# Kernel tuning notes

Measured on AMD Instinct MI355X. Metric: run time of the kernel, lower is better.

Reference implementation:

```python
import jax, jax.numpy as jnp
import numpy as np

N_NODES = 50000
N_EDGES = 800000
VOCAB = 4096          # node_emb_size
EMB_DIM = 128         # node_emb_dim
HIDDEN = 128          # hidden_dim -> layer1 out = 2*HIDDEN
N_POS = 1024


def gcn_conv(h, edge_index, W, b, n):
    """PyG GCNConv: lin -> add self loops -> sym-normalized scatter-add -> +bias."""
    h = h @ W                                   # [N, out]
    row, col = edge_index[0], edge_index[1]     # source, target
    loop = jnp.arange(n)
    row = jnp.concatenate([row, loop])
    col = jnp.concatenate([col, loop])
    deg = jax.ops.segment_sum(jnp.ones(row.shape[0], dtype=h.dtype), col, num_segments=n)
    dinv = jnp.where(deg > 0, jax.lax.rsqrt(deg), 0.0)
    norm = dinv[row] * dinv[col]                # [E+N]
    msg = h[row] * norm[:, None]                # gather + scale
    return jax.ops.segment_sum(msg, col, num_segments=n) + b


def setup_inputs() -> dict:
    key = jax.random.key(0)
    ks = jax.random.split(key, 10)
    x = jax.random.randint(ks[0], (N_NODES, 1), 0, VOCAB)
    edge_index = jax.random.randint(ks[1], (2, N_EDGES), 0, N_NODES)
    x_position = jax.random.randint(ks[2], (N_POS,), 0, N_NODES)
    # Embedding init: normal(0, emb_dim^-0.5) per initialize_parameters
    emb = jax.random.normal(ks[3], (VOCAB, EMB_DIM), jnp.float32) * EMB_DIM ** -0.5
    # GCN / linear weights (glorot-ish)
    W1 = jax.random.normal(ks[4], (EMB_DIM, 2 * HIDDEN), jnp.float32) * (EMB_DIM ** -0.5)
    b1 = jnp.zeros((2 * HIDDEN,), jnp.float32)
    W2 = jax.random.normal(ks[5], (2 * HIDDEN, HIDDEN), jnp.float32) * ((2 * HIDDEN) ** -0.5)
    b2 = jnp.zeros((HIDDEN,), jnp.float32)
    Wc = jax.random.normal(ks[6], (HIDDEN, VOCAB), jnp.float32) * (HIDDEN ** -0.5)
    bc = jnp.zeros((VOCAB,), jnp.float32)
    return {"x": x, "edge_index": edge_index, "x_position": x_position,
            "emb": emb, "W1": W1, "b1": b1, "W2": W2, "b2": b2, "Wc": Wc, "bc": bc}


def reference(x, edge_index, x_position, emb, W1, b1, W2, b2, Wc, bc):
    n = x.shape[0]
    h = emb[x[:, 0]]                                   # Embedding + squeeze(1)
    h = jax.nn.relu(gcn_conv(h, edge_index, W1, b1, n))
    z = gcn_conv(h, edge_index, W2, b2, n)             # [N, HIDDEN]
    logits = z @ Wc + bc                               # classifier over all nodes
    # embedding stage: mean of classified rows at x_position, keep dim 0
    return jnp.mean(logits[x_position], axis=0, keepdims=True)  # [1, VOCAB]
```

## Files before the change

kernel.cpp:

```cpp
#include <hip/hip_runtime.h>

constexpr int EMB  = 128;
constexpr int H1D  = 256;
constexpr int H2D  = 128;
constexpr int VOC  = 4096;
constexpr int NSL  = 32;
constexpr int RPB  = 4;

constexpr int NRANGE = 8;
constexpr int TEAMS  = 128;
constexpr int RCAP   = 6400;
constexpr int HIST_B = NRANGE * TEAMS;
constexpr int GEMM_B = VOC / RPB;
constexpr int KB_GRID = HIST_B + GEMM_B;

__global__ void kA_init(int* count, unsigned int* flagbits, unsigned int* needw,
                        float* wagg, float* wsum, int* nflag, int* total,
                        const int* __restrict__ xpos,
                        int n, int nwords, int np) {
    int t = threadIdx.x;
    if (blockIdx.x == 0) {
        for (int i = t; i < nwords; i += 256) flagbits[i] = 0u;
        for (int i = t; i < n; i += 256) count[i] = 0;
        __syncthreads();
        for (int i = t; i < np; i += 256) {
            int v = xpos[i];
            atomicAdd(&count[v], 1);
            atomicOr(&flagbits[v >> 5], 1u << (v & 31));
        }
        if (t == 0) { *nflag = 0; *total = 0; }
    } else {
        const int stride = (gridDim.x - 1) * 256;
        const int i0 = (blockIdx.x - 1) * 256 + t;
        for (int i = i0; i < n; i += stride) wagg[i] = 0.0f;
        for (int i = i0; i < nwords; i += stride) needw[i] = 0u;
        for (int i = i0; i < NSL * H1D; i += stride) wsum[i] = 0.0f;
    }
}

__global__ __launch_bounds__(256) void kB_embW1_hist(
        const float* __restrict__ emb, const float* __restrict__ W1,
        float* __restrict__ embW1,
        const int* __restrict__ row, const int* __restrict__ col,
        const unsigned int* __restrict__ flagbits,
        unsigned short* __restrict__ cntp16, unsigned int* markw,
        int ne, int R, int sTeam) {
    __shared__ int sbuf[RCAP];
    int t = threadIdx.x;
    if (blockIdx.x < HIST_B) {
        int h     = blockIdx.x;
        int team  = h >> 3;
        int range = h & (NRANGE - 1);
        int base  = range * R;
        for (int i = t; i < R; i += 256) sbuf[i] = 0;
        __syncthreads();
        int q  = (((ne + TEAMS - 1) / TEAMS) + 255) & ~255;
        int e0 = team * q;
        int e1 = min(ne, e0 + q);
        for (int e = e0 + t; e < e1; e += 256) {
            int c = col[e];
            unsigned int d = (unsigned int)(c - base);
            if (d < (unsigned int)R) {
                atomicAdd(&sbuf[d], 1);
                if ((flagbits[c >> 5] >> (c & 31)) & 1u) {
                    int r = row[e];
                    atomicOr(&markw[r >> 5], 1u << (r & 31));
                }
            }
        }
        __syncthreads();
        unsigned short* outp = cntp16 + (size_t)team * sTeam + base;
        for (int i = t; i < R; i += 256) outp[i] = (unsigned short)sbuf[i];
    } else {
        float (*er)[EMB] = (float (*)[EMB])sbuf;
        int r0 = (blockIdx.x - HIST_B) * RPB;
        for (int i = t; i < RPB * EMB; i += 256)
            er[i / EMB][i % EMB] = emb[(size_t)r0 * EMB + i];
        __syncthreads();
        float acc[RPB];
#pragma unroll
        for (int rr = 0; rr < RPB; rr++) acc[rr] = 0.0f;
        for (int k = 0; k < EMB; k++) {
            float w = W1[k * H1D + t];
#pragma unroll
            for (int rr = 0; rr < RPB; rr++) acc[rr] += er[rr][k] * w;
        }
#pragma unroll
        for (int rr = 0; rr < RPB; rr++)
            embW1[(size_t)(r0 + rr) * H1D + t] = acc[rr];
    }
}

__global__ void k_alloc(unsigned int* needw,
                        const unsigned int* __restrict__ flagbits,
                        const unsigned short* __restrict__ cntp16,
                        const int* __restrict__ count,
                        const int* __restrict__ x,
                        float* wagg, int* needlist, int* nflag, int* total,
                        int* offs, int* cursor, int2* pk, int* cnt,
                        int n, int sTeam) {
    int v = blockIdx.x * blockDim.x + threadIdx.x;
    int lane = threadIdx.x & 63;
    int cv = 0;
    bool need = false;
    if (v < n) {
        const unsigned short* cp = cntp16 + v;
#pragma unroll 8
        for (int tt = 0; tt < TEAMS; tt++) cv += cp[(size_t)tt * sTeam];
        cnt[v] = cv;
        float dv = rsqrtf((float)cv + 1.0f);
        int2 p; p.x = x[v]; p.y = __float_as_int(dv);
        pk[v] = p;
        bool mark = (needw[v >> 5] >> (v & 31)) & 1u;
        bool flag = (flagbits[v >> 5] >> (v & 31)) & 1u;
        need = mark || flag;
        if (flag) wagg[v] = (float)count[v] / ((float)cv + 1.0f);
    }
    unsigned long long nm = __ballot(need);
    int wbase = (v & ~63) >> 5;
    if (lane == 0)  needw[wbase]     = (unsigned int)(nm & 0xffffffffu);
    if (lane == 32) needw[wbase + 1] = (unsigned int)(nm >> 32);
    int seg = need ? cv : 0;
    int incl = seg;
#pragma unroll
    for (int d = 1; d < 64; d <<= 1) {
        int t2 = __shfl_up(incl, d);
        if (lane >= d) incl += t2;
    }
    int excl = incl - seg;
    int wave_total = __shfl(incl, 63);
    int rank = __popcll(nm & ((1ull << lane) - 1));
    int wcnt = __popcll(nm);
    int base_id = 0, base_off = 0;
    if (lane == 0) {
        if (wcnt > 0)       base_id  = atomicAdd(nflag, wcnt);
        if (wave_total > 0) base_off = atomicAdd(total, wave_total);
    }
    base_id  = __shfl(base_id, 0);
    base_off = __shfl(base_off, 0);
    if (need) {
        needlist[base_id + rank] = v;
        int o = base_off + excl;
        offs[v] = o;
        cursor[v] = o;
    }
}

__global__ void k_scatter(const int* __restrict__ row, const int* __restrict__ col,
                          const unsigned int* __restrict__ needw,
                          const unsigned int* __restrict__ flagbits,
                          const int* __restrict__ count,
                          const int2* __restrict__ pk,
                          int* cursor, int2* srowp, float* wagg, int ne) {
    int e = blockIdx.x * blockDim.x + threadIdx.x;
    if (e < ne) {
        int c = col[e];
        if ((needw[c >> 5] >> (c & 31)) & 1u) {
            int r = row[e];
            int pos = atomicAdd(&cursor[c], 1);
            int2 pr = pk[r];
            srowp[pos] = pr;
            if ((flagbits[c >> 5] >> (c & 31)) & 1u) {
                float dc = __int_as_float(pk[c].y);
                float dr = __int_as_float(pr.y);
                atomicAdd(&wagg[r], (float)count[c] * dc * dr);
            }
        }
    }
}

__global__ void k_fconv(const int* __restrict__ needlist, const int* __restrict__ nneed_p,
                        const float* __restrict__ wagg, const int* __restrict__ x,
                        const int2* __restrict__ srowp,
                        const int* __restrict__ offs, const int* __restrict__ cnt,
                        const float* __restrict__ embW1, const float* __restrict__ b1,
                        float* __restrict__ wsum) {
    int lane = threadIdx.x & 63;
    int wib  = threadIdx.x >> 6;
    int wid  = blockIdx.x * (blockDim.x >> 6) + wib;
    int nw   = gridDim.x * (blockDim.x >> 6);
    int nn   = *nneed_p;
    const float4* __restrict__ ew = (const float4*)embW1;
    float4 bfrag = ((const float4*)b1)[lane];
    float4 acc2 = {0.0f, 0.0f, 0.0f, 0.0f};

    for (int i = wid; i < nn; i += nw) {
        int v = needlist[i];
        int cv = cnt[v];
        float dv = rsqrtf((float)cv + 1.0f);
        float wa = wagg[v];
        float4 s = ew[(size_t)x[v] * 64 + lane];
        float w0 = dv * dv;
        float4 acc;
        acc.x = bfrag.x + w0 * s.x;
        acc.y = bfrag.y + w0 * s.y;
        acc.z = bfrag.z + w0 * s.z;
        acc.w = bfrag.w + w0 * s.w;
        int start = offs[v], m = cv;
        for (int base = 0; base < m; base += 64) {
            int mm = min(64, m - base);
            int xr = 0; float wr = 0.0f;
            if (lane < mm) {
                int2 pk2 = srowp[start + base + lane];
                xr = pk2.x;
                wr = __int_as_float(pk2.y) * dv;
            }
            int e = 0;
            for (; e + 4 <= mm; e += 4) {
                int i0 = __shfl(xr, e),     i1 = __shfl(xr, e + 1);
                int i2 = __shfl(xr, e + 2), i3 = __shfl(xr, e + 3);
                float q0 = __shfl(wr, e),     q1 = __shfl(wr, e + 1);
                float q2 = __shfl(wr, e + 2), q3 = __shfl(wr, e + 3);
                float4 t0 = ew[(size_t)i0 * 64 + lane];
                float4 t1 = ew[(size_t)i1 * 64 + lane];
                float4 t2 = ew[(size_t)i2 * 64 + lane];
                float4 t3 = ew[(size_t)i3 * 64 + lane];
                acc.x += q0 * t0.x + q1 * t1.x + q2 * t2.x + q3 * t3.x;
                acc.y += q0 * t0.y + q1 * t1.y + q2 * t2.y + q3 * t3.y;
                acc.z += q0 * t0.z + q1 * t1.z + q2 * t2.z + q3 * t3.z;
                acc.w += q0 * t0.w + q1 * t1.w + q2 * t2.w + q3 * t3.w;
            }
            for (; e < mm; e++) {
                int i0 = __shfl(xr, e);
                float q0 = __shfl(wr, e);
                float4 t0 = ew[(size_t)i0 * 64 + lane];
                acc.x += q0 * t0.x;
                acc.y += q0 * t0.y;
                acc.z += q0 * t0.z;
                acc.w += q0 * t0.w;
            }
        }
        acc2.x += wa * fmaxf(acc.x, 0.0f);
        acc2.y += wa * fmaxf(acc.y, 0.0f);
        acc2.z += wa * fmaxf(acc.z, 0.0f);
        acc2.w += wa * fmaxf(acc.w, 0.0f);
    }

    __shared__ float red[4][H1D];
    red[wib][4 * lane + 0] = acc2.x;
    red[wib][4 * lane + 1] = acc2.y;
    red[wib][4 * lane + 2] = acc2.z;
    red[wib][4 * lane + 3] = acc2.w;
    __syncthreads();
    int t = threadIdx.x;
    float ssum = red[0][t] + red[1][t] + red[2][t] + red[3][t];
    atomicAdd(&wsum[(blockIdx.x & (NSL - 1)) * H1D + t], ssum);
}

__global__ void k_zout(const float* __restrict__ wsum, const float* __restrict__ W2,
                       const float* __restrict__ b2, const float* __restrict__ Wc,
                       const float* __restrict__ bc, float* __restrict__ out,
                       float inv_np) {
    __shared__ float ws[H1D];
    __shared__ float z[H2D];
    __shared__ float red[256];
    int t = threadIdx.x;
    float s = 0.0f;
#pragma unroll
    for (int c2 = 0; c2 < NSL; c2++) s += wsum[c2 * H1D + t];
    ws[t] = s;
    __syncthreads();
    if (t < H2D) {
        float acc = 0.0f;
#pragma unroll 8
        for (int k = 0; k < H1D; k++) acc += ws[k] * W2[k * H2D + t];
        z[t] = b2[t] + acc * inv_np;
    }
    __syncthreads();
    int c  = blockIdx.x * 64 + (t & 63);
    int ks = t >> 6;
    float acc = 0.0f;
#pragma unroll 8
    for (int j = ks * 32; j < ks * 32 + 32; j++) acc += z[j] * Wc[(size_t)j * VOC + c];
    red[t] = acc;
    __syncthreads();
    if (t < 64) {
        int cc = blockIdx.x * 64 + t;
        out[cc] = bc[cc] + red[t] + red[t + 64] + red[t + 128] + red[t + 192];
    }
}

extern "C" void kernel_launch(void* const* d_in, const int* in_sizes, int n_in,
                              void* d_out, int out_size, void* d_ws, size_t ws_size,
                              hipStream_t stream) {
    const int n  = in_sizes[0];
    const int ne = in_sizes[1] / 2;
    const int np = in_sizes[2];

    const int*   x    = (const int*)d_in[0];
    const int*   ei   = (const int*)d_in[1];
    const int*   xpos = (const int*)d_in[2];
    const float* emb  = (const float*)d_in[3];
    const float* W1   = (const float*)d_in[4];
    const float* b1   = (const float*)d_in[5];
    const float* W2   = (const float*)d_in[6];
    const float* b2   = (const float*)d_in[7];
    const float* Wc   = (const float*)d_in[8];
    const float* bc   = (const float*)d_in[9];
    float*       out  = (float*)d_out;

    const int* row = ei;
    const int* col = ei + ne;

    char* p = (char*)d_ws;
    auto alloc = [&](size_t bytes) {
        char* r = p;
        p += (bytes + 255) & ~(size_t)255;
        return r;
    };
    const int nb     = (n + 255) / 256;
    const int neb    = (ne + 255) / 256;
    const int nwords = nb * 8;
    const int R      = (n + NRANGE - 1) / NRANGE;
    const int sTeam  = NRANGE * R;

    int*            cnt      = (int*)alloc((size_t)n * 4);
    int*            offs     = (int*)alloc((size_t)n * 4);
    int*            cursor   = (int*)alloc((size_t)n * 4);
    int*            count    = (int*)alloc((size_t)n * 4);
    int*            needlist = (int*)alloc((size_t)n * 4);
    unsigned int*   needw    = (unsigned int*)alloc((size_t)nwords * 4);
    unsigned int*   flagbits = (unsigned int*)alloc((size_t)nwords * 4);
    int2*           srowp    = (int2*)alloc((size_t)ne * 8);
    int2*           pk       = (int2*)alloc((size_t)n * 8);
    unsigned short* cntp16   = (unsigned short*)alloc((size_t)TEAMS * sTeam * 2);
    int*            nflag    = (int*)alloc(256 * 4);
    int*            total    = (int*)alloc(256 * 4);
    float*          wagg     = (float*)alloc((size_t)n * 4);
    float*          embW1    = (float*)alloc((size_t)VOC * H1D * 4);
    float*          wsum     = (float*)alloc((size_t)NSL * H1D * 4);

    kA_init<<<nb, 256, 0, stream>>>(count, flagbits, needw, wagg, wsum,
                                    nflag, total, xpos, n, nwords, np);
    kB_embW1_hist<<<KB_GRID, 256, 0, stream>>>(emb, W1, embW1, row, col, flagbits,
                                               cntp16, needw, ne, R, sTeam);
    k_alloc<<<nb, 256, 0, stream>>>(needw, flagbits, cntp16, count, x, wagg,
                                    needlist, nflag, total, offs, cursor, pk, cnt,
                                    n, sTeam);
    k_scatter<<<neb, 256, 0, stream>>>(row, col, needw, flagbits, count, pk,
                                       cursor, srowp, wagg, ne);
    k_fconv<<<2048, 256, 0, stream>>>(needlist, nflag, wagg, x, srowp, offs, cnt,
                                      embW1, b1, wsum);
    k_zout<<<VOC / 64, 256, 0, stream>>>(wsum, W2, b2, Wc, bc, out, 1.0f / (float)np);
}
```

Measured before the change: 169.7 us.

## Pack histogram counters and edge payloads to 16-bit, halve teams, widen zout grid

The histogram now packs two 16-bit counters per shared-memory word with half as many teams, which halves the LDS footprint and the partial-count traffic. Per-node records shrink from int2 (vocab id plus dinv float) to one 32-bit word holding a 16-bit degree and a 16-bit vocab id, and dinv is recomputed with rsqrtf where needed. This halves gather and scatter bandwidth, but it assumes vocab ids and per-team counts fit in 16 bits. The classifier kernel is launched with 4x more blocks, each handling 16 columns, to raise parallelism over the Wc read.

New measurement: 179.2 us. 5.6% more time.

```diff
diff --git a/kernel.cpp b/kernel.cpp
--- a/kernel.cpp
+++ b/kernel.cpp
@@ -8,8 +8,8 @@
 constexpr int RPB  = 4;
 
 constexpr int NRANGE = 8;
-constexpr int TEAMS  = 128;
-constexpr int RCAP   = 6400;
+constexpr int TEAMS  = 64;
+constexpr int RCAPW  = 3200;
 constexpr int HIST_B = NRANGE * TEAMS;
 constexpr int GEMM_B = VOC / RPB;
 constexpr int KB_GRID = HIST_B + GEMM_B;
@@ -45,14 +45,15 @@
         const unsigned int* __restrict__ flagbits,
         unsigned short* __restrict__ cntp16, unsigned int* markw,
         int ne, int R, int sTeam) {
-    __shared__ int sbuf[RCAP];
+    __shared__ unsigned int sbuf[RCAPW];
     int t = threadIdx.x;
     if (blockIdx.x < HIST_B) {
         int h     = blockIdx.x;
         int team  = h >> 3;
         int range = h & (NRANGE - 1);
         int base  = range * R;
-        for (int i = t; i < R; i += 256) sbuf[i] = 0;
+        int RW    = R >> 1;
+        for (int i = t; i < RW; i += 256) sbuf[i] = 0u;
         __syncthreads();
         int q  = (((ne + TEAMS - 1) / TEAMS) + 255) & ~255;
         int e0 = team * q;
@@ -61,7 +62,7 @@
             int c = col[e];
             unsigned int d = (unsigned int)(c - base);
             if (d < (unsigned int)R) {
-                atomicAdd(&sbuf[d], 1);
+                atomicAdd(&sbuf[d >> 1], 1u << ((d & 1) << 4));
                 if ((flagbits[c >> 5] >> (c & 31)) & 1u) {
                     int r = row[e];
                     atomicOr(&markw[r >> 5], 1u << (r & 31));
@@ -69,8 +70,9 @@
             }
         }
         __syncthreads();
-        unsigned short* outp = cntp16 + (size_t)team * sTeam + base;
-        for (int i = t; i < R; i += 256) outp[i] = (unsigned short)sbuf[i];
+        unsigned int* outp32 =
+            (unsigned int*)(cntp16 + (size_t)team * sTeam + base);
+        for (int i = t; i < RW; i += 256) outp32[i] = sbuf[i];
     } else {
         float (*er)[EMB] = (float (*)[EMB])sbuf;
         int r0 = (blockIdx.x - HIST_B) * RPB;
@@ -97,7 +99,7 @@
                         const int* __restrict__ count,
                         const int* __restrict__ x,
                         float* wagg, int* needlist, int* nflag, int* total,
-                        int* offs, int* cursor, int2* pk, int* cnt,
+                        int* offs, int* cursor, unsigned int* pkc, int* cnt,
                         int n, int sTeam) {
     int v = blockIdx.x * blockDim.x + threadIdx.x;
     int lane = threadIdx.x & 63;
@@ -108,9 +110,7 @@
 #pragma unroll 8
         for (int tt = 0; tt < TEAMS; tt++) cv += cp[(size_t)tt * sTeam];
         cnt[v] = cv;
-        float dv = rsqrtf((float)cv + 1.0f);
-        int2 p; p.x = x[v]; p.y = __float_as_int(dv);
-        pk[v] = p;
+        pkc[v] = ((unsigned int)cv << 16) | (unsigned int)(x[v] & 0xFFFF);
         bool mark = (needw[v >> 5] >> (v & 31)) & 1u;
         bool flag = (flagbits[v >> 5] >> (v & 31)) & 1u;
         need = mark || flag;
@@ -150,19 +150,19 @@
                           const unsigned int* __restrict__ needw,
                           const unsigned int* __restrict__ flagbits,
                           const int* __restrict__ count,
-                          const int2* __restrict__ pk,
-                          int* cursor, int2* srowp, float* wagg, int ne) {
+                          const unsigned int* __restrict__ pkc,
+                          int* cursor, unsigned int* srow4, float* wagg, int ne) {
     int e = blockIdx.x * blockDim.x + threadIdx.x;
     if (e < ne) {
         int c = col[e];
         if ((needw[c >> 5] >> (c & 31)) & 1u) {
             int r = row[e];
             int pos = atomicAdd(&cursor[c], 1);
-            int2 pr = pk[r];
-            srowp[pos] = pr;
+            unsigned int pr = pkc[r];
+            srow4[pos] = pr;
             if ((flagbits[c >> 5] >> (c & 31)) & 1u) {
-                float dc = __int_as_float(pk[c].y);
-                float dr = __int_as_float(pr.y);
+                float dr = rsqrtf((float)(pr >> 16) + 1.0f);
+                float dc = rsqrtf((float)(pkc[c] >> 16) + 1.0f);
                 atomicAdd(&wagg[r], (float)count[c] * dc * dr);
             }
         }
@@ -171,7 +171,7 @@
 
 __global__ void k_fconv(const int* __restrict__ needlist, const int* __restrict__ nneed_p,
                         const float* __restrict__ wagg, const int* __restrict__ x,
-                        const int2* __restrict__ srowp,
+                        const unsigned int* __restrict__ srow4,
                         const int* __restrict__ offs, const int* __restrict__ cnt,
                         const float* __restrict__ embW1, const float* __restrict__ b1,
                         float* __restrict__ wsum) {
@@ -201,9 +201,9 @@
             int mm = min(64, m - base);
             int xr = 0; float wr = 0.0f;
             if (lane < mm) {
-                int2 pk2 = srowp[start + base + lane];
-                xr = pk2.x;
-                wr = __int_as_float(pk2.y) * dv;
+                unsigned int pk2 = srow4[start + base + lane];
+                xr = (int)(pk2 & 0xFFFFu);
+                wr = rsqrtf((float)(pk2 >> 16) + 1.0f) * dv;
             }
             int e = 0;
             for (; e + 4 <= mm; e += 4) {
@@ -267,16 +267,19 @@
         z[t] = b2[t] + acc * inv_np;
     }
     __syncthreads();
-    int c  = blockIdx.x * 64 + (t & 63);
-    int ks = t >> 6;
+    int c  = blockIdx.x * 16 + (t & 15);
+    int js = t >> 4;
     float acc = 0.0f;
-#pragma unroll 8
-    for (int j = ks * 32; j < ks * 32 + 32; j++) acc += z[j] * Wc[(size_t)j * VOC + c];
+#pragma unroll
+    for (int j = js * 8; j < js * 8 + 8; j++) acc += z[j] * Wc[(size_t)j * VOC + c];
     red[t] = acc;
     __syncthreads();
-    if (t < 64) {
-        int cc = blockIdx.x * 64 + t;
-        out[cc] = bc[cc] + red[t] + red[t + 64] + red[t + 128] + red[t + 192];
+    if (t < 16) {
+        int cc = blockIdx.x * 16 + t;
+        float o = bc[cc];
+#pragma unroll
+        for (int ss = 0; ss < 16; ss++) o += red[ss * 16 + t];
+        out[cc] = o;
     }
 }
 
@@ -311,7 +314,7 @@
     const int nb     = (n + 255) / 256;
     const int neb    = (ne + 255) / 256;
     const int nwords = nb * 8;
-    const int R      = (n + NRANGE - 1) / NRANGE;
+    const int R      = (((n + NRANGE - 1) / NRANGE) + 1) & ~1;
     const int sTeam  = NRANGE * R;
 
     int*            cnt      = (int*)alloc((size_t)n * 4);
@@ -321,8 +324,8 @@
     int*            needlist = (int*)alloc((size_t)n * 4);
     unsigned int*   needw    = (unsigned int*)alloc((size_t)nwords * 4);
     unsigned int*   flagbits = (unsigned int*)alloc((size_t)nwords * 4);
-    int2*           srowp    = (int2*)alloc((size_t)ne * 8);
-    int2*           pk       = (int2*)alloc((size_t)n * 8);
+    unsigned int*   srow4    = (unsigned int*)alloc((size_t)ne * 4);
+    unsigned int*   pkc      = (unsigned int*)alloc((size_t)n * 4);
     unsigned short* cntp16   = (unsigned short*)alloc((size_t)TEAMS * sTeam * 2);
     int*            nflag    = (int*)alloc(256 * 4);
     int*            total    = (int*)alloc(256 * 4);
@@ -335,11 +338,11 @@
     kB_embW1_hist<<<KB_GRID, 256, 0, stream>>>(emb, W1, embW1, row, col, flagbits,
                                                cntp16, needw, ne, R, sTeam);
     k_alloc<<<nb, 256, 0, stream>>>(needw, flagbits, cntp16, count, x, wagg,
-                                    needlist, nflag, total, offs, cursor, pk, cnt,
+                                    needlist, nflag, total, offs, cursor, pkc, cnt,
                                     n, sTeam);
-    k_scatter<<<neb, 256, 0, stream>>>(row, col, needw, flagbits, count, pk,
-                                       cursor, srowp, wagg, ne);
-    k_fconv<<<2048, 256, 0, stream>>>(needlist, nflag, wagg, x, srowp, offs, cnt,
+    k_scatter<<<neb, 256, 0, stream>>>(row, col, needw, flagbits, count, pkc,
+                                       cursor, srow4, wagg, ne);
+    k_fconv<<<2048, 256, 0, stream>>>(needlist, nflag, wagg, x, srow4, offs, cnt,
                                       embW1, b1, wsum);
-    k_zout<<<VOC / 64, 256, 0, stream>>>(wsum, W2, b2, Wc, bc, out, 1.0f / (float)np);
-}
+    k_zout<<<VOC / 16, 256, 0, stream>>>(wsum, W2, b2, Wc, bc, out, 1.0f / (float)np);
+}
```
